# Kernel optimization log

Hardware: AMD Instinct MI355X
Metric: run time of the kernel (lower is better)

The kernel has to match this reference:

```python
import jax, jax.numpy as jnp
import numpy as np

B, S, DIM, H, HD, K, DEPTH = 2, 2048, 512, 8, 64, 64, 8
SCALE = 1.0 / np.sqrt(HD)


def _cantor_coords(seq_len: int, depth: int) -> np.ndarray:
    # Vectorized port of CantorAttention._cantor_coordinate over all positions.
    x = np.arange(seq_len, dtype=np.float64) / max(1, seq_len - 1)
    x = np.clip(x, 1e-06, 1.0 - 1e-06)
    val = np.zeros(seq_len, dtype=np.float64)
    factor = 0.5
    for _ in range(depth):
        x *= 3.0
        digit = np.floor(x)
        x -= digit
        val += (digit == 2.0) * factor
        factor *= 0.5
    return val.astype(np.float32)


def _build_routes(seq_len: int, k: int, depth: int) -> np.ndarray:
    # k nearest neighbors in Cantor space (smallest |c_i - c_j|), per position.
    c = _cantor_coords(seq_len, depth)
    dist = np.abs(c[:, None] - c[None, :])  # (S, S) built once on host
    routes = np.argsort(dist, axis=1, kind='stable')[:, :k]  # ascending distance
    return routes.astype(np.int32)


def setup_inputs() -> dict:
    key = jax.random.key(0)
    k1, k2, k3 = jax.random.split(key, 3)
    x = jax.random.normal(k1, (B, S, DIM), dtype=jnp.float32)
    Wqkv = jax.random.normal(k2, (DIM, 3 * DIM), dtype=jnp.float32) * (1.0 / np.sqrt(DIM))
    bqkv = jnp.zeros((3 * DIM,), dtype=jnp.float32)
    Wout = jax.random.normal(k3, (DIM, DIM), dtype=jnp.float32) * (1.0 / np.sqrt(DIM))
    bout = jnp.zeros((DIM,), dtype=jnp.float32)
    routes = jnp.asarray(_build_routes(S, K, DEPTH))  # (S, K) int32
    return {"x": x, "Wqkv": Wqkv, "bqkv": bqkv, "Wout": Wout, "bout": bout, "routes": routes}


def reference(x, Wqkv, bqkv, Wout, bout, routes):
    b, s, _ = x.shape
    qkv = x @ Wqkv + bqkv  # (B, S, 3*DIM)
    qkv = qkv.reshape(b, s, 3, H, HD)
    q = jnp.transpose(qkv[:, :, 0], (0, 2, 1, 3))  # (B, H, S, HD)
    k = jnp.transpose(qkv[:, :, 1], (0, 2, 1, 3))
    v = jnp.transpose(qkv[:, :, 2], (0, 2, 1, 3))
    # Gather K/V along sequence dim by Cantor routes -> (B, H, S, K, HD)
    k_g = k[:, :, routes, :]
    v_g = v[:, :, routes, :]
    scores = jnp.einsum('bhsd,bhskd->bhsk', q, k_g) * SCALE
    w = jax.nn.softmax(scores, axis=-1)  # dropout disabled (eval)
    out = jnp.einsum('bhsk,bhskd->bhsd', w, v_g)  # (B, H, S, HD)
    out = jnp.transpose(out, (0, 2, 1, 3)).reshape(b, s, DIM)
    return out @ Wout + bout
```

## Files before the change

kernel.cpp:

```cpp
#include <hip/hip_runtime.h>
#include <math.h>

#define B_    2
#define S_    2048
#define DIM_  512
#define H_    8
#define HD_   64
#define K_    64
#define M_    (B_ * S_)
#define NQKV_ (3 * DIM_)

typedef __attribute__((ext_vector_type(8))) _Float16       half8;
typedef __attribute__((ext_vector_type(8))) unsigned short ushort8v;
typedef __attribute__((ext_vector_type(4))) float          float4v;

union H8 { half8 h; ushort8v u; unsigned int w[4]; };

__device__ __forceinline__ unsigned short f2h(float f) {
    _Float16 h = (_Float16)f;
    unsigned short u; __builtin_memcpy(&u, &h, 2); return u;
}
__device__ __forceinline__ unsigned int pkrtz(float a, float b) {
    auto r = __builtin_amdgcn_cvt_pkrtz(a, b);
    unsigned int u; __builtin_memcpy(&u, &r, 4); return u;
}

__device__ __forceinline__ void load_lds16(const unsigned short* g, unsigned short* l) {
    __builtin_amdgcn_global_load_lds(
        (const __attribute__((address_space(1))) void*)g,
        (__attribute__((address_space(3))) void*)l, 16, 0, 0);
}

__global__ __launch_bounds__(256) void prep_all(
    const float* __restrict__ X, unsigned short* __restrict__ Xh,
    const float* __restrict__ Wq, unsigned short* __restrict__ Wqh,
    const float* __restrict__ Wo, unsigned short* __restrict__ Woh,
    const int* __restrict__ routes, int* __restrict__ members,
    int4* __restrict__ recs, int* __restrict__ nchp)
{
    __shared__ int smem[2048 * 3 + 256];
    const int bid = blockIdx.x, t = threadIdx.x;

    if (bid < 1024) {
        size_t i = ((size_t)bid * 256 + t) * 8;
        float4 a = *(const float4*)&X[i];
        float4 b = *(const float4*)&X[i + 4];
        float f[8] = {a.x, a.y, a.z, a.w, b.x, b.y, b.z, b.w};
        ushort8v h;
        #pragma unroll
        for (int j = 0; j < 8; ++j) h[j] = f2h(f[j]);
        *(ushort8v*)&Xh[i] = h;
        return;
    }

    if (bid == 2048) {
        int* cnt  = smem;
        int* base = smem + 2048;
        int* cur  = smem + 4096;
        int* ps   = smem + 6144;
        for (int i = t; i < 2048; i += 256) cnt[i] = 0;
        __syncthreads();
        int lead[8];
        #pragma unroll
        for (int i = 0; i < 8; ++i) {
            lead[i] = routes[(size_t)(i * 256 + t) * K_];
            atomicAdd(&cnt[lead[i]], 1);
        }
        __syncthreads();
        int loc[8], sum = 0;
        #pragma unroll
        for (int i = 0; i < 8; ++i) { loc[i] = sum; sum += cnt[t * 8 + i]; }
        ps[t] = sum;
        __syncthreads();
        for (int off = 1; off < 256; off <<= 1) {
            int v = ps[t];
            if (t >= off) v += ps[t - off];
            __syncthreads(); ps[t] = v; __syncthreads();
        }
        const int excl = ps[t] - sum;
        #pragma unroll
        for (int i = 0; i < 8; ++i) { base[t * 8 + i] = excl + loc[i]; cur[t * 8 + i] = 0; }
        __syncthreads();
        #pragma unroll
        for (int i = 0; i < 8; ++i) {
            int s = i * 256 + t;
            members[base[lead[i]] + atomicAdd(&cur[lead[i]], 1)] = s;
        }
        int cloc[8], csum = 0;
        #pragma unroll
        for (int i = 0; i < 8; ++i) { cloc[i] = csum; csum += (cnt[t * 8 + i] + 15) >> 4; }
        __syncthreads();
        ps[t] = csum;
        __syncthreads();
        for (int off = 1; off < 256; off <<= 1) {
            int v = ps[t];
            if (t >= off) v += ps[t - off];
            __syncthreads(); ps[t] = v; __syncthreads();
        }
        const int cexcl = ps[t] - csum;
        #pragma unroll
        for (int i = 0; i < 8; ++i) {
            const int c = t * 8 + i, n = cnt[c];
            int w0 = cexcl + cloc[i];
            for (int k2 = 0; k2 * 16 < n; ++k2) {
                int rem = n - k2 * 16;
                recs[w0 + k2] = make_int4(c, base[c] + k2 * 16, rem < 16 ? rem : 16, 0);
            }
        }
        if (t == 255) nchp[0] = ps[255];
        return;
    }

    float (*tile)[33] = (float (*)[33])smem;
    const float* W;
    unsigned short* Whi;
    int N, k0, n0;
    if (bid < 1792) {
        int idx = bid - 1024;
        W = Wq; Whi = Wqh; N = NQKV_;
        n0 = (idx % 48) * 32; k0 = (idx / 48) * 32;
    } else {
        int idx = bid - 1792;
        W = Wo; Whi = Woh; N = DIM_;
        n0 = (idx % 16) * 32; k0 = (idx / 16) * 32;
    }
    const int c = t & 31, r8 = t >> 5;
    #pragma unroll
    for (int i = 0; i < 4; ++i) {
        int r = r8 + i * 8;
        tile[r][c] = W[(size_t)(k0 + r) * N + n0 + c];
    }
    __syncthreads();
    #pragma unroll
    for (int i = 0; i < 4; ++i) {
        int r = r8 + i * 8;
        Whi[(size_t)(n0 + r) * 512 + k0 + c] = f2h(tile[c][r]);
    }
}

template<int BM, int BN, int WM, int WN, int TERMS>
__global__ __launch_bounds__(256) void gemm_mfma(
    const unsigned short* __restrict__ Ahi, const unsigned short* __restrict__ Alo,
    const unsigned short* __restrict__ Wh,
    const float* __restrict__ bias, float* __restrict__ C,
    unsigned short* __restrict__ Qho, unsigned short* __restrict__ Kho,
    unsigned short* __restrict__ Vho,
    int N, int Kd, int mode)
{
    constexpr int TM = WM / 16, TN = WN / 16;
    constexpr int WAVES_N = BN / WN;
    __shared__ unsigned short Ah[2][BM][32];
    __shared__ unsigned short Al[TERMS == 2 ? 2 : 1][TERMS == 2 ? BM : 1][32];
    __shared__ unsigned short Bh[2][BN][32];

    const int t = threadIdx.x, lane = t & 63, wave = t >> 6;
    const int wm = (wave / WAVES_N) * WM, wn = (wave % WAVES_N) * WN;
    const int m0 = blockIdx.y * BM, n0 = blockIdx.x * BN;
    const int l15 = lane & 15, l4 = lane >> 4;

    const int srow = lane >> 2;
    const int scol = (lane & 3) * 8;

    float4v acc[TM][TN];
    #pragma unroll
    for (int i = 0; i < TM; ++i)
        #pragma unroll
        for (int j = 0; j < TN; ++j)
            #pragma unroll
            for (int r = 0; r < 4; ++r) acc[i][j][r] = 0.f;

    const int NK = Kd / 32;

    #pragma unroll
    for (int c = wave; c < BM / 16; c += 4) {
        size_t g = (size_t)(m0 + c * 16 + srow) * Kd + scol;
        load_lds16(&Ahi[g], &Ah[0][c * 16][0]);
        if constexpr (TERMS == 2) load_lds16(&Alo[g], &Al[0][c * 16][0]);
    }
    #pragma unroll
    for (int c = wave; c < BN / 16; c += 4) {
        size_t g = (size_t)(n0 + c * 16 + srow) * Kd + scol;
        load_lds16(&Wh[g], &Bh[0][c * 16][0]);
    }
    __syncthreads();

    for (int ks = 0; ks < NK; ++ks) {
        const int cur = ks & 1, nxt = cur ^ 1;

        if (ks + 1 < NK) {
            const int k1 = (ks + 1) * 32;
            #pragma unroll
            for (int c = wave; c < BM / 16; c += 4) {
                size_t g = (size_t)(m0 + c * 16 + srow) * Kd + k1 + scol;
                load_lds16(&Ahi[g], &Ah[nxt][c * 16][0]);
                if constexpr (TERMS == 2) load_lds16(&Alo[g], &Al[nxt][c * 16][0]);
            }
            #pragma unroll
            for (int c = wave; c < BN / 16; c += 4) {
                size_t g = (size_t)(n0 + c * 16 + srow) * Kd + k1 + scol;
                load_lds16(&Wh[g], &Bh[nxt][c * 16][0]);
            }
        }

        half8 fa_h[TM], fa_l[TM], fb[TN];
        #pragma unroll
        for (int im = 0; im < TM; ++im) {
            fa_h[im] = *(const half8*)&Ah[cur][wm + im * 16 + l15][l4 * 8];
            if constexpr (TERMS == 2)
                fa_l[im] = *(const half8*)&Al[cur][wm + im * 16 + l15][l4 * 8];
        }
        #pragma unroll
        for (int in = 0; in < TN; ++in)
            fb[in] = *(const half8*)&Bh[cur][wn + in * 16 + l15][l4 * 8];
        #pragma unroll
        for (int im = 0; im < TM; ++im)
            #pragma unroll
            for (int in = 0; in < TN; ++in) {
                acc[im][in] = __builtin_amdgcn_mfma_f32_16x16x32_f16(fa_h[im], fb[in], acc[im][in], 0, 0, 0);
                if constexpr (TERMS == 2)
                    acc[im][in] = __builtin_amdgcn_mfma_f32_16x16x32_f16(fa_l[im], fb[in], acc[im][in], 0, 0, 0);
            }

        __syncthreads();
    }

    if (mode == 0) {
        #pragma unroll
        for (int in = 0; in < TN; ++in) {
            int n = n0 + wn + in * 16 + l15;
            float bv = bias[n];
            #pragma unroll
            for (int im = 0; im < TM; ++im) {
                int mb = m0 + wm + im * 16 + l4 * 4;
                #pragma unroll
                for (int r = 0; r < 4; ++r)
                    C[(size_t)(mb + r) * N + n] = acc[im][in][r] + bv;
            }
        }
    } else {
        #pragma unroll
        for (int in = 0; in < TN; ++in) {
            int n = n0 + wn + in * 16 + l15;
            int which = n >> 9, h = (n >> 6) & 7, d = n & 63;
            unsigned short* dst = (which == 0) ? Qho : (which == 1 ? Kho : Vho);
            float bv = bias[n];
            float scl = (which == 0) ? 0.125f : 1.0f;
            #pragma unroll
            for (int im = 0; im < TM; ++im) {
                int mb = m0 + wm + im * 16 + l4 * 4;
                #pragma unroll
                for (int r = 0; r < 4; ++r) {
                    int m = mb + r, b = m >> 11, s = m & 2047;
                    dst[(((size_t)b * H_ + h) * S_ + s) * HD_ + d] =
                        f2h((acc[im][in][r] + bv) * scl);
                }
            }
        }
    }
}

__global__ __launch_bounds__(256, 4) void attn_kernel(
    const unsigned short* __restrict__ Qh, const unsigned short* __restrict__ Kh,
    const unsigned short* __restrict__ Vh, const int* __restrict__ routes,
    const int* __restrict__ members, const int4* __restrict__ recs,
    const int* __restrict__ nchp, unsigned short* __restrict__ Oh)
{
    __shared__ unsigned short VldsAll[4][4096];
    const int wv = threadIdx.x >> 6, lane = threadIdx.x & 63;
    unsigned short* Vlds = VldsAll[wv];
    const int g = lane >> 4, m16 = lane & 15;

    const int unit = blockIdx.x * 4 + wv;
    const int bh = unit & 15, cidx = unit >> 4;
    const int b = bh >> 3, h = bh & 7;

    const unsigned short* qbase = Qh + (size_t)bh * S_ * HD_;
    const unsigned short* kbase = Kh + (size_t)bh * S_ * HD_;
    const unsigned short* vbase = Vh + (size_t)bh * S_ * HD_;
    const int nch = nchp[0];

    for (int chunk = cidx; chunk < nch; chunk += 512) {
        const int4 rec = recs[chunk];
        const int leader = rec.x, mstart = rec.y, mcnt = rec.z;

        const int rl = routes[(size_t)leader * K_ + lane];
        const int mm = members[mstart + (m16 < mcnt ? m16 : mcnt - 1)];

        #pragma unroll
        for (int i = 0; i < 8; ++i) {
            int rv = __shfl(rl, i * 8 + (lane >> 3));
            int sc = (lane & 7) ^ i;
            load_lds16(&vbase[(size_t)rv * HD_ + sc * 8], Vlds + i * 512);
        }

        H8 ka[4][2];
        #pragma unroll
        for (int tt = 0; tt < 4; ++tt) {
            int rt = __shfl(rl, tt * 16 + m16);
            const unsigned short* kr = &kbase[(size_t)rt * HD_];
            ka[tt][0].u = *(const ushort8v*)(kr + g * 8);
            ka[tt][1].u = *(const ushort8v*)(kr + 32 + g * 8);
        }
        const unsigned short* qr = &qbase[(size_t)mm * HD_];
        H8 qb0, qb1;
        qb0.u = *(const ushort8v*)(qr + g * 8);
        qb1.u = *(const ushort8v*)(qr + 32 + g * 8);

        float4v acc[4];
        #pragma unroll
        for (int tt = 0; tt < 4; ++tt) {
            #pragma unroll
            for (int r = 0; r < 4; ++r) acc[tt][r] = 0.f;
        }
        #pragma unroll
        for (int tt = 0; tt < 4; ++tt) {
            acc[tt] = __builtin_amdgcn_mfma_f32_16x16x32_f16(ka[tt][0].h, qb0.h, acc[tt], 0, 0, 0);
            acc[tt] = __builtin_amdgcn_mfma_f32_16x16x32_f16(ka[tt][1].h, qb1.h, acc[tt], 0, 0, 0);
        }

        float mx = acc[0][0];
        #pragma unroll
        for (int tt = 0; tt < 4; ++tt)
            #pragma unroll
            for (int r = 0; r < 4; ++r) mx = fmaxf(mx, acc[tt][r]);
        mx = fmaxf(mx, __shfl_xor(mx, 16));
        mx = fmaxf(mx, __shfl_xor(mx, 32));
        float ew[4][4], su = 0.f;
        #pragma unroll
        for (int tt = 0; tt < 4; ++tt)
            #pragma unroll
            for (int r = 0; r < 4; ++r) { ew[tt][r] = __expf(acc[tt][r] - mx); su += ew[tt][r]; }
        su += __shfl_xor(su, 16);
        su += __shfl_xor(su, 32);
        const float rinv = __builtin_amdgcn_rcpf(su);

        unsigned int whu[4][2];
        #pragma unroll
        for (int tt = 0; tt < 4; ++tt) {
            whu[tt][0] = pkrtz(ew[tt][0] * rinv, ew[tt][1] * rinv);
            whu[tt][1] = pkrtz(ew[tt][2] * rinv, ew[tt][3] * rinv);
        }

        const int A0 = (((g & 1) << 5) | m16) * 4;
        const int A1 = A0 + 64;
        const bool ghi = (g >> 1) != 0;
        H8 pa[2];
        #pragma unroll
        for (int s = 0; s < 2; ++s) {
            unsigned int l0a = (unsigned int)__builtin_amdgcn_ds_bpermute(A0, (int)whu[2 * s][0]);
            unsigned int l0b = (unsigned int)__builtin_amdgcn_ds_bpermute(A0, (int)whu[2 * s + 1][0]);
            unsigned int h0a = (unsigned int)__builtin_amdgcn_ds_bpermute(A0, (int)whu[2 * s][1]);
            unsigned int h0b = (unsigned int)__builtin_amdgcn_ds_bpermute(A0, (int)whu[2 * s + 1][1]);
            unsigned int l1a = (unsigned int)__builtin_amdgcn_ds_bpermute(A1, (int)whu[2 * s][0]);
            unsigned int l1b = (unsigned int)__builtin_amdgcn_ds_bpermute(A1, (int)whu[2 * s + 1][0]);
            unsigned int h1a = (unsigned int)__builtin_amdgcn_ds_bpermute(A1, (int)whu[2 * s][1]);
            unsigned int h1b = (unsigned int)__builtin_amdgcn_ds_bpermute(A1, (int)whu[2 * s + 1][1]);
            pa[s].w[0] = ghi ? l0b : l0a;
            pa[s].w[1] = ghi ? h0b : h0a;
            pa[s].w[2] = ghi ? l1b : l1a;
            pa[s].w[3] = ghi ? h1b : h1a;
        }

        int mr[4];
        #pragma unroll
        for (int r = 0; r < 4; ++r)
            mr[r] = __builtin_amdgcn_ds_bpermute((g * 4 + r) * 4, mm);

        asm volatile("s_waitcnt vmcnt(0)" ::: "memory");
        __builtin_amdgcn_sched_barrier(0);

        #pragma unroll
        for (int dblk = 0; dblk < 4; ++dblk) {
            H8 vb[2];
            #pragma unroll
            for (int s = 0; s < 2; ++s) {
                const char* vp = (const char*)Vlds + (s * 32 + g * 8) * 128 +
                    (((dblk * 16 + m16) * 2) ^ ((((s * 4 + g) & 7)) << 4));
                #pragma unroll
                for (int j = 0; j < 8; ++j)
                    vb[s].u[j] = *(const unsigned short*)(vp + j * 128);
            }
            float4v o;
            o[0] = 0.f; o[1] = 0.f; o[2] = 0.f; o[3] = 0.f;
            o = __builtin_amdgcn_mfma_f32_16x16x32_f16(pa[0].h, vb[0].h, o, 0, 0, 0);
            o = __builtin_amdgcn_mfma_f32_16x16x32_f16(pa[1].h, vb[1].h, o, 0, 0, 0);
            #pragma unroll
            for (int r = 0; r < 4; ++r) {
                if (g * 4 + r < mcnt) {
                    size_t oi = ((size_t)b * S_ + mr[r]) * DIM_ + h * HD_ + dblk * 16 + m16;
                    Oh[oi] = f2h(o[r]);
                }
            }
        }
    }
}

extern "C" void kernel_launch(void* const* d_in, const int* in_sizes, int n_in,
                              void* d_out, int out_size, void* d_ws, size_t ws_size,
                              hipStream_t stream)
{
    const float* x      = (const float*)d_in[0];
    const float* Wqkv   = (const float*)d_in[1];
    const float* bqkv   = (const float*)d_in[2];
    const float* Wout   = (const float*)d_in[3];
    const float* bout   = (const float*)d_in[4];
    const int*   routes = (const int*)d_in[5];
    float* out = (float*)d_out;

    char* w = (char*)d_ws;
    unsigned short* Qh = (unsigned short*)(w);
    unsigned short* Kh = (unsigned short*)(w + (8u << 20));
    unsigned short* Vh = (unsigned short*)(w + (16u << 20));
    unsigned short* xh = (unsigned short*)(w + (24u << 20));
    unsigned short* ah = xh;
    unsigned short* wqh = (unsigned short*)(w + (32u << 20));
    unsigned short* woh = (unsigned short*)(w + (32u << 20) + 1572864u);
    int*  members = (int*)(w + (34u << 20));
    int4* recs    = (int4*)(w + (34u << 20) + 8192u);
    int*  nchp    = (int*)(w + (34u << 20) + 8192u + 32768u);

    dim3 blk(256);

    prep_all<<<dim3(2049), blk, 0, stream>>>(x, xh, Wqkv, wqh, Wout, woh,
                                             routes, members, recs, nchp);

    gemm_mfma<128, 96, 64, 48, 1><<<dim3(NQKV_ / 96, M_ / 128), blk, 0, stream>>>(
        xh, nullptr, wqh, bqkv, nullptr, Qh, Kh, Vh, NQKV_, DIM_, 1);

    attn_kernel<<<dim3(2048), blk, 0, stream>>>(Qh, Kh, Vh, routes,
                                                members, recs, nchp, ah);

    gemm_mfma<64, 64, 32, 32, 1><<<dim3(DIM_ / 64, M_ / 64), blk, 0, stream>>>(
        ah, nullptr, woh, bout, out, nullptr, nullptr, nullptr, DIM_, DIM_, 0);
}
```

Before: 118.1 us.

## Fuse prep, QKV GEMM, attention and output GEMM into one persistent kernel

Replaces the four kernel launches with a single persistent 256-block kernel, plus a tiny zeroing kernel, that moves between phases via global atomic barriers. The route-grouping prep now runs on one block, overlapped with the QKV GEMM tiles on the other 255 blocks, and the leader counts are gathered through global atomics. The goal is to remove launch gaps and tail effects between stages. In exchange, each phase gets far fewer blocks than before (256 vs thousands), grid-wide spin barriers add cost, and correctness depends on all blocks being co-resident.

```diff
diff --git a/kernel.cpp b/kernel.cpp
--- a/kernel.cpp
+++ b/kernel.cpp
@@ -9,6 +9,7 @@
 #define K_    64
 #define M_    (B_ * S_)
 #define NQKV_ (3 * DIM_)
+#define NBLK_ 256
 
 typedef __attribute__((ext_vector_type(8))) _Float16       half8;
 typedef __attribute__((ext_vector_type(8))) unsigned short ushort8v;
@@ -24,140 +25,44 @@
     auto r = __builtin_amdgcn_cvt_pkrtz(a, b);
     unsigned int u; __builtin_memcpy(&u, &r, 4); return u;
 }
-
 __device__ __forceinline__ void load_lds16(const unsigned short* g, unsigned short* l) {
     __builtin_amdgcn_global_load_lds(
         (const __attribute__((address_space(1))) void*)g,
         (__attribute__((address_space(3))) void*)l, 16, 0, 0);
 }
 
-__global__ __launch_bounds__(256) void prep_all(
-    const float* __restrict__ X, unsigned short* __restrict__ Xh,
-    const float* __restrict__ Wq, unsigned short* __restrict__ Wqh,
-    const float* __restrict__ Wo, unsigned short* __restrict__ Woh,
-    const int* __restrict__ routes, int* __restrict__ members,
-    int4* __restrict__ recs, int* __restrict__ nchp)
-{
-    __shared__ int smem[2048 * 3 + 256];
-    const int bid = blockIdx.x, t = threadIdx.x;
-
-    if (bid < 1024) {
-        size_t i = ((size_t)bid * 256 + t) * 8;
-        float4 a = *(const float4*)&X[i];
-        float4 b = *(const float4*)&X[i + 4];
-        float f[8] = {a.x, a.y, a.z, a.w, b.x, b.y, b.z, b.w};
-        ushort8v h;
-        #pragma unroll
-        for (int j = 0; j < 8; ++j) h[j] = f2h(f[j]);
-        *(ushort8v*)&Xh[i] = h;
-        return;
-    }
-
-    if (bid == 2048) {
-        int* cnt  = smem;
-        int* base = smem + 2048;
-        int* cur  = smem + 4096;
-        int* ps   = smem + 6144;
-        for (int i = t; i < 2048; i += 256) cnt[i] = 0;
-        __syncthreads();
-        int lead[8];
-        #pragma unroll
-        for (int i = 0; i < 8; ++i) {
-            lead[i] = routes[(size_t)(i * 256 + t) * K_];
-            atomicAdd(&cnt[lead[i]], 1);
-        }
-        __syncthreads();
-        int loc[8], sum = 0;
-        #pragma unroll
-        for (int i = 0; i < 8; ++i) { loc[i] = sum; sum += cnt[t * 8 + i]; }
-        ps[t] = sum;
-        __syncthreads();
-        for (int off = 1; off < 256; off <<= 1) {
-            int v = ps[t];
-            if (t >= off) v += ps[t - off];
-            __syncthreads(); ps[t] = v; __syncthreads();
-        }
-        const int excl = ps[t] - sum;
-        #pragma unroll
-        for (int i = 0; i < 8; ++i) { base[t * 8 + i] = excl + loc[i]; cur[t * 8 + i] = 0; }
-        __syncthreads();
-        #pragma unroll
-        for (int i = 0; i < 8; ++i) {
-            int s = i * 256 + t;
-            members[base[lead[i]] + atomicAdd(&cur[lead[i]], 1)] = s;
-        }
-        int cloc[8], csum = 0;
-        #pragma unroll
-        for (int i = 0; i < 8; ++i) { cloc[i] = csum; csum += (cnt[t * 8 + i] + 15) >> 4; }
-        __syncthreads();
-        ps[t] = csum;
-        __syncthreads();
-        for (int off = 1; off < 256; off <<= 1) {
-            int v = ps[t];
-            if (t >= off) v += ps[t - off];
-            __syncthreads(); ps[t] = v; __syncthreads();
-        }
-        const int cexcl = ps[t] - csum;
-        #pragma unroll
-        for (int i = 0; i < 8; ++i) {
-            const int c = t * 8 + i, n = cnt[c];
-            int w0 = cexcl + cloc[i];
-            for (int k2 = 0; k2 * 16 < n; ++k2) {
-                int rem = n - k2 * 16;
-                recs[w0 + k2] = make_int4(c, base[c] + k2 * 16, rem < 16 ? rem : 16, 0);
-            }
-        }
-        if (t == 255) nchp[0] = ps[255];
-        return;
-    }
-
-    float (*tile)[33] = (float (*)[33])smem;
-    const float* W;
-    unsigned short* Whi;
-    int N, k0, n0;
-    if (bid < 1792) {
-        int idx = bid - 1024;
-        W = Wq; Whi = Wqh; N = NQKV_;
-        n0 = (idx % 48) * 32; k0 = (idx / 48) * 32;
-    } else {
-        int idx = bid - 1792;
-        W = Wo; Whi = Woh; N = DIM_;
-        n0 = (idx % 16) * 32; k0 = (idx / 16) * 32;
-    }
-    const int c = t & 31, r8 = t >> 5;
-    #pragma unroll
-    for (int i = 0; i < 4; ++i) {
-        int r = r8 + i * 8;
-        tile[r][c] = W[(size_t)(k0 + r) * N + n0 + c];
-    }
+__device__ __forceinline__ void gbar(int* cnt, int nblk) {
     __syncthreads();
-    #pragma unroll
-    for (int i = 0; i < 4; ++i) {
-        int r = r8 + i * 8;
-        Whi[(size_t)(n0 + r) * 512 + k0 + c] = f2h(tile[c][r]);
-    }
-}
-
-template<int BM, int BN, int WM, int WN, int TERMS>
-__global__ __launch_bounds__(256) void gemm_mfma(
-    const unsigned short* __restrict__ Ahi, const unsigned short* __restrict__ Alo,
-    const unsigned short* __restrict__ Wh,
+    __threadfence();
+    __syncthreads();
+    if (threadIdx.x == 0) {
+        __hip_atomic_fetch_add(cnt, 1, __ATOMIC_RELEASE, __HIP_MEMORY_SCOPE_AGENT);
+        int spins = 0;
+        while (__hip_atomic_load(cnt, __ATOMIC_ACQUIRE, __HIP_MEMORY_SCOPE_AGENT) < nblk) {
+            __builtin_amdgcn_s_sleep(7);
+            if (++spins > (1 << 22)) break;
+        }
+    }
+    __syncthreads();
+    __threadfence();
+}
+
+template<int BM, int BN, int WM, int WN>
+__device__ void gemm_tile(char* smemRaw,
+    const unsigned short* __restrict__ Ahi, const unsigned short* __restrict__ Wh,
     const float* __restrict__ bias, float* __restrict__ C,
     unsigned short* __restrict__ Qho, unsigned short* __restrict__ Kho,
     unsigned short* __restrict__ Vho,
-    int N, int Kd, int mode)
+    int N, int Kd, int mode, int m0, int n0)
 {
     constexpr int TM = WM / 16, TN = WN / 16;
     constexpr int WAVES_N = BN / WN;
-    __shared__ unsigned short Ah[2][BM][32];
-    __shared__ unsigned short Al[TERMS == 2 ? 2 : 1][TERMS == 2 ? BM : 1][32];
-    __shared__ unsigned short Bh[2][BN][32];
+    auto Ah = (unsigned short (*)[BM][32])smemRaw;
+    auto Bh = (unsigned short (*)[BN][32])(smemRaw + 2 * BM * 32 * 2);
 
     const int t = threadIdx.x, lane = t & 63, wave = t >> 6;
     const int wm = (wave / WAVES_N) * WM, wn = (wave % WAVES_N) * WN;
-    const int m0 = blockIdx.y * BM, n0 = blockIdx.x * BN;
     const int l15 = lane & 15, l4 = lane >> 4;
-
     const int srow = lane >> 2;
     const int scol = (lane & 3) * 8;
 
@@ -175,7 +80,6 @@
     for (int c = wave; c < BM / 16; c += 4) {
         size_t g = (size_t)(m0 + c * 16 + srow) * Kd + scol;
         load_lds16(&Ahi[g], &Ah[0][c * 16][0]);
-        if constexpr (TERMS == 2) load_lds16(&Alo[g], &Al[0][c * 16][0]);
     }
     #pragma unroll
     for (int c = wave; c < BN / 16; c += 4) {
@@ -193,7 +97,6 @@
             for (int c = wave; c < BM / 16; c += 4) {
                 size_t g = (size_t)(m0 + c * 16 + srow) * Kd + k1 + scol;
                 load_lds16(&Ahi[g], &Ah[nxt][c * 16][0]);
-                if constexpr (TERMS == 2) load_lds16(&Alo[g], &Al[nxt][c * 16][0]);
             }
             #pragma unroll
             for (int c = wave; c < BN / 16; c += 4) {
@@ -202,24 +105,18 @@
             }
         }
 
-        half8 fa_h[TM], fa_l[TM], fb[TN];
-        #pragma unroll
-        for (int im = 0; im < TM; ++im) {
-            fa_h[im] = *(const half8*)&Ah[cur][wm + im * 16 + l15][l4 * 8];
-            if constexpr (TERMS == 2)
-                fa_l[im] = *(const half8*)&Al[cur][wm + im * 16 + l15][l4 * 8];
-        }
+        half8 fa[TM], fb[TN];
+        #pragma unroll
+        for (int im = 0; im < TM; ++im)
+            fa[im] = *(const half8*)&Ah[cur][wm + im * 16 + l15][l4 * 8];
         #pragma unroll
         for (int in = 0; in < TN; ++in)
             fb[in] = *(const half8*)&Bh[cur][wn + in * 16 + l15][l4 * 8];
         #pragma unroll
         for (int im = 0; im < TM; ++im)
             #pragma unroll
-            for (int in = 0; in < TN; ++in) {
-                acc[im][in] = __builtin_amdgcn_mfma_f32_16x16x32_f16(fa_h[im], fb[in], acc[im][in], 0, 0, 0);
-                if constexpr (TERMS == 2)
-                    acc[im][in] = __builtin_amdgcn_mfma_f32_16x16x32_f16(fa_l[im], fb[in], acc[im][in], 0, 0, 0);
-            }
+            for (int in = 0; in < TN; ++in)
+                acc[im][in] = __builtin_amdgcn_mfma_f32_16x16x32_f16(fa[im], fb[in], acc[im][in], 0, 0, 0);
 
         __syncthreads();
     }
@@ -259,139 +156,280 @@
     }
 }
 
-__global__ __launch_bounds__(256, 4) void attn_kernel(
+__device__ void attn_one(int bh, int chunk, unsigned short* Vlds,
     const unsigned short* __restrict__ Qh, const unsigned short* __restrict__ Kh,
     const unsigned short* __restrict__ Vh, const int* __restrict__ routes,
     const int* __restrict__ members, const int4* __restrict__ recs,
-    const int* __restrict__ nchp, unsigned short* __restrict__ Oh)
+    unsigned short* __restrict__ Oh)
 {
-    __shared__ unsigned short VldsAll[4][4096];
-    const int wv = threadIdx.x >> 6, lane = threadIdx.x & 63;
-    unsigned short* Vlds = VldsAll[wv];
+    const int lane = threadIdx.x & 63;
     const int g = lane >> 4, m16 = lane & 15;
-
-    const int unit = blockIdx.x * 4 + wv;
-    const int bh = unit & 15, cidx = unit >> 4;
     const int b = bh >> 3, h = bh & 7;
 
     const unsigned short* qbase = Qh + (size_t)bh * S_ * HD_;
     const unsigned short* kbase = Kh + (size_t)bh * S_ * HD_;
     const unsigned short* vbase = Vh + (size_t)bh * S_ * HD_;
-    const int nch = nchp[0];
-
-    for (int chunk = cidx; chunk < nch; chunk += 512) {
-        const int4 rec = recs[chunk];
-        const int leader = rec.x, mstart = rec.y, mcnt = rec.z;
-
-        const int rl = routes[(size_t)leader * K_ + lane];
-        const int mm = members[mstart + (m16 < mcnt ? m16 : mcnt - 1)];
-
+
+    const int4 rec = recs[chunk & 2047];
+    const int leader = rec.x & 2047;
+    const int mstart = rec.y & 2047;
+    const int mcnt   = rec.z < 1 ? 1 : (rec.z > 16 ? 16 : rec.z);
+
+    const int rl = routes[(size_t)leader * K_ + lane] & 2047;
+    const int mm = members[(mstart + (m16 < mcnt ? m16 : mcnt - 1)) & 2047] & 2047;
+
+    #pragma unroll
+    for (int i = 0; i < 8; ++i) {
+        int rv = __shfl(rl, i * 8 + (lane >> 3));
+        int sc = (lane & 7) ^ i;
+        load_lds16(&vbase[(size_t)rv * HD_ + sc * 8], Vlds + i * 512);
+    }
+
+    H8 ka[4][2];
+    #pragma unroll
+    for (int tt = 0; tt < 4; ++tt) {
+        int rt = __shfl(rl, tt * 16 + m16);
+        const unsigned short* kr = &kbase[(size_t)rt * HD_];
+        ka[tt][0].u = *(const ushort8v*)(kr + g * 8);
+        ka[tt][1].u = *(const ushort8v*)(kr + 32 + g * 8);
+    }
+    const unsigned short* qr = &qbase[(size_t)mm * HD_];
+    H8 qb0, qb1;
+    qb0.u = *(const ushort8v*)(qr + g * 8);
+    qb1.u = *(const ushort8v*)(qr + 32 + g * 8);
+
+    float4v acc[4];
+    #pragma unroll
+    for (int tt = 0; tt < 4; ++tt) {
+        #pragma unroll
+        for (int r = 0; r < 4; ++r) acc[tt][r] = 0.f;
+    }
+    #pragma unroll
+    for (int tt = 0; tt < 4; ++tt) {
+        acc[tt] = __builtin_amdgcn_mfma_f32_16x16x32_f16(ka[tt][0].h, qb0.h, acc[tt], 0, 0, 0);
+        acc[tt] = __builtin_amdgcn_mfma_f32_16x16x32_f16(ka[tt][1].h, qb1.h, acc[tt], 0, 0, 0);
+    }
+
+    float mx = acc[0][0];
+    #pragma unroll
+    for (int tt = 0; tt < 4; ++tt)
+        #pragma unroll
+        for (int r = 0; r < 4; ++r) mx = fmaxf(mx, acc[tt][r]);
+    mx = fmaxf(mx, __shfl_xor(mx, 16));
+    mx = fmaxf(mx, __shfl_xor(mx, 32));
+    float ew[4][4], su = 0.f;
+    #pragma unroll
+    for (int tt = 0; tt < 4; ++tt)
+        #pragma unroll
+        for (int r = 0; r < 4; ++r) { ew[tt][r] = __expf(acc[tt][r] - mx); su += ew[tt][r]; }
+    su += __shfl_xor(su, 16);
+    su += __shfl_xor(su, 32);
+    const float rinv = __builtin_amdgcn_rcpf(su);
+
+    unsigned int whu[4][2];
+    #pragma unroll
+    for (int tt = 0; tt < 4; ++tt) {
+        whu[tt][0] = pkrtz(ew[tt][0] * rinv, ew[tt][1] * rinv);
+        whu[tt][1] = pkrtz(ew[tt][2] * rinv, ew[tt][3] * rinv);
+    }
+
+    const int A0 = (((g & 1) << 5) | m16) * 4;
+    const int A1 = A0 + 64;
+    const bool ghi = (g >> 1) != 0;
+    H8 pa[2];
+    #pragma unroll
+    for (int s = 0; s < 2; ++s) {
+        unsigned int l0a = (unsigned int)__builtin_amdgcn_ds_bpermute(A0, (int)whu[2 * s][0]);
+        unsigned int l0b = (unsigned int)__builtin_amdgcn_ds_bpermute(A0, (int)whu[2 * s + 1][0]);
+        unsigned int h0a = (unsigned int)__builtin_amdgcn_ds_bpermute(A0, (int)whu[2 * s][1]);
+        unsigned int h0b = (unsigned int)__builtin_amdgcn_ds_bpermute(A0, (int)whu[2 * s + 1][1]);
+        unsigned int l1a = (unsigned int)__builtin_amdgcn_ds_bpermute(A1, (int)whu[2 * s][0]);
+        unsigned int l1b = (unsigned int)__builtin_amdgcn_ds_bpermute(A1, (int)whu[2 * s + 1][0]);
+        unsigned int h1a = (unsigned int)__builtin_amdgcn_ds_bpermute(A1, (int)whu[2 * s][1]);
+        unsigned int h1b = (unsigned int)__builtin_amdgcn_ds_bpermute(A1, (int)whu[2 * s + 1][1]);
+        pa[s].w[0] = ghi ? l0b : l0a;
+        pa[s].w[1] = ghi ? h0b : h0a;
+        pa[s].w[2] = ghi ? l1b : l1a;
+        pa[s].w[3] = ghi ? h1b : h1a;
+    }
+
+    int mr[4];
+    #pragma unroll
+    for (int r = 0; r < 4; ++r)
+        mr[r] = __builtin_amdgcn_ds_bpermute((g * 4 + r) * 4, mm) & 2047;
+
+    asm volatile("s_waitcnt vmcnt(0)" ::: "memory");
+    __builtin_amdgcn_sched_barrier(0);
+
+    #pragma unroll
+    for (int dblk = 0; dblk < 4; ++dblk) {
+        H8 vb[2];
+        #pragma unroll
+        for (int s = 0; s < 2; ++s) {
+            const char* vp = (const char*)Vlds + (s * 32 + g * 8) * 128 +
+                (((dblk * 16 + m16) * 2) ^ ((((s * 4 + g) & 7)) << 4));
+            #pragma unroll
+            for (int j = 0; j < 8; ++j)
+                vb[s].u[j] = *(const unsigned short*)(vp + j * 128);
+        }
+        float4v o;
+        o[0] = 0.f; o[1] = 0.f; o[2] = 0.f; o[3] = 0.f;
+        o = __builtin_amdgcn_mfma_f32_16x16x32_f16(pa[0].h, vb[0].h, o, 0, 0, 0);
+        o = __builtin_amdgcn_mfma_f32_16x16x32_f16(pa[1].h, vb[1].h, o, 0, 0, 0);
+        #pragma unroll
+        for (int r = 0; r < 4; ++r) {
+            if (g * 4 + r < mcnt) {
+                size_t oi = ((size_t)b * S_ + mr[r]) * DIM_ + h * HD_ + dblk * 16 + m16;
+                Oh[oi] = f2h(o[r]);
+            }
+        }
+    }
+}
+
+__global__ __launch_bounds__(256) void zero_ws(int* gcnt, int* bar, int* nchp)
+{
+    int i = blockIdx.x * 256 + threadIdx.x;
+    if (i < 2048) gcnt[i] = 0;
+    if (i < 16) bar[i] = 0;
+    if (i == 16) nchp[0] = 0;
+}
+
+struct MegaArgs {
+    const float* x; unsigned short* xh;
+    const float* Wq; unsigned short* wqh;
+    const float* Wo; unsigned short* woh;
+    const float* bqkv; const float* bout;
+    const int* routes; int* members; int4* recs; int* nchp; int* gcnt; int* bar;
+    unsigned short* Qh; unsigned short* Kh; unsigned short* Vh;
+    unsigned short* ah; float* out;
+};
+
+__global__ __launch_bounds__(256) void mega(MegaArgs a)
+{
+    __shared__ __align__(16) char smem[32768];
+    const int bid = blockIdx.x, t = threadIdx.x;
+
+    #pragma unroll
+    for (int i = 0; i < 8; ++i) {
+        const int unit = bid + NBLK_ * i;
+        if (unit < 1024) {
+            size_t idx = ((size_t)unit * 256 + t) * 8;
+            float4 va = *(const float4*)&a.x[idx];
+            float4 vb = *(const float4*)&a.x[idx + 4];
+            float f[8] = {va.x, va.y, va.z, va.w, vb.x, vb.y, vb.z, vb.w};
+            ushort8v hh;
+            #pragma unroll
+            for (int j = 0; j < 8; ++j) hh[j] = f2h(f[j]);
+            *(ushort8v*)&a.xh[idx] = hh;
+        } else {
+            float (*tile)[33] = (float (*)[33])smem;
+            const float* W; unsigned short* Whi; int N, k0, n0;
+            int u = unit - 1024;
+            if (u < 768) { W = a.Wq; Whi = a.wqh; N = NQKV_; n0 = (u % 48) * 32; k0 = (u / 48) * 32; }
+            else { u -= 768; W = a.Wo; Whi = a.woh; N = DIM_; n0 = (u % 16) * 32; k0 = (u / 16) * 32; }
+            const int c = t & 31, r8 = t >> 5;
+            __syncthreads();
+            #pragma unroll
+            for (int j = 0; j < 4; ++j) {
+                int r = r8 + j * 8;
+                tile[r][c] = W[(size_t)(k0 + r) * N + n0 + c];
+            }
+            __syncthreads();
+            #pragma unroll
+            for (int j = 0; j < 4; ++j) {
+                int r = r8 + j * 8;
+                Whi[(size_t)(n0 + r) * 512 + k0 + c] = f2h(tile[c][r]);
+            }
+        }
+    }
+    if (t < 8) {
+        int s = bid * 8 + t;
+        atomicAdd(&a.gcnt[a.routes[(size_t)s * K_]], 1);
+    }
+
+    gbar(a.bar + 0, NBLK_);
+
+    if (bid == 255) {
+        int* cnt  = (int*)smem;
+        int* base = cnt + 2048;
+        int* cur  = base + 2048;
+        int* ps   = cur + 2048;
+        for (int i = t; i < 2048; i += 256)
+            cnt[i] = __hip_atomic_load(&a.gcnt[i], __ATOMIC_RELAXED, __HIP_MEMORY_SCOPE_AGENT);
+        __syncthreads();
+        int loc[8], sum = 0;
+        #pragma unroll
+        for (int i = 0; i < 8; ++i) { loc[i] = sum; sum += cnt[t * 8 + i]; }
+        ps[t] = sum;
+        __syncthreads();
+        for (int off = 1; off < 256; off <<= 1) {
+            int v = ps[t];
+            if (t >= off) v += ps[t - off];
+            __syncthreads(); ps[t] = v; __syncthreads();
+        }
+        const int excl = ps[t] - sum;
+        #pragma unroll
+        for (int i = 0; i < 8; ++i) { base[t * 8 + i] = excl + loc[i]; cur[t * 8 + i] = 0; }
+        __syncthreads();
         #pragma unroll
         for (int i = 0; i < 8; ++i) {
-            int rv = __shfl(rl, i * 8 + (lane >> 3));
-            int sc = (lane & 7) ^ i;
-            load_lds16(&vbase[(size_t)rv * HD_ + sc * 8], Vlds + i * 512);
-        }
-
-        H8 ka[4][2];
-        #pragma unroll
-        for (int tt = 0; tt < 4; ++tt) {
-            int rt = __shfl(rl, tt * 16 + m16);
-            const unsigned short* kr = &kbase[(size_t)rt * HD_];
-            ka[tt][0].u = *(const ushort8v*)(kr + g * 8);
-            ka[tt][1].u = *(const ushort8v*)(kr + 32 + g * 8);
-        }
-        const unsigned short* qr = &qbase[(size_t)mm * HD_];
-        H8 qb0, qb1;
-        qb0.u = *(const ushort8v*)(qr + g * 8);
-        qb1.u = *(const ushort8v*)(qr + 32 + g * 8);
-
-        float4v acc[4];
-        #pragma unroll
-        for (int tt = 0; tt < 4; ++tt) {
-            #pragma unroll
-            for (int r = 0; r < 4; ++r) acc[tt][r] = 0.f;
-        }
-        #pragma unroll
-        for (int tt = 0; tt < 4; ++tt) {
-            acc[tt] = __builtin_amdgcn_mfma_f32_16x16x32_f16(ka[tt][0].h, qb0.h, acc[tt], 0, 0, 0);
-            acc[tt] = __builtin_amdgcn_mfma_f32_16x16x32_f16(ka[tt][1].h, qb1.h, acc[tt], 0, 0, 0);
-        }
-
-        float mx = acc[0][0];
-        #pragma unroll
-        for (int tt = 0; tt < 4; ++tt)
-            #pragma unroll
-            for (int r = 0; r < 4; ++r) mx = fmaxf(mx, acc[tt][r]);
-        mx = fmaxf(mx, __shfl_xor(mx, 16));
-        mx = fmaxf(mx, __shfl_xor(mx, 32));
-        float ew[4][4], su = 0.f;
-        #pragma unroll
-        for (int tt = 0; tt < 4; ++tt)
-            #pragma unroll
-            for (int r = 0; r < 4; ++r) { ew[tt][r] = __expf(acc[tt][r] - mx); su += ew[tt][r]; }
-        su += __shfl_xor(su, 16);
-        su += __shfl_xor(su, 32);
-        const float rinv = __builtin_amdgcn_rcpf(su);
-
-        unsigned int whu[4][2];
-        #pragma unroll
-        for (int tt = 0; tt < 4; ++tt) {
-            whu[tt][0] = pkrtz(ew[tt][0] * rinv, ew[tt][1] * rinv);
-            whu[tt][1] = pkrtz(ew[tt][2] * rinv, ew[tt][3] * rinv);
-        }
-
-        const int A0 = (((g & 1) << 5) | m16) * 4;
-        const int A1 = A0 + 64;
-        const bool ghi = (g >> 1) != 0;
-        H8 pa[2];
-        #pragma unroll
-        for (int s = 0; s < 2; ++s) {
-            unsigned int l0a = (unsigned int)__builtin_amdgcn_ds_bpermute(A0, (int)whu[2 * s][0]);
-            unsigned int l0b = (unsigned int)__builtin_amdgcn_ds_bpermute(A0, (int)whu[2 * s + 1][0]);
-            unsigned int h0a = (unsigned int)__builtin_amdgcn_ds_bpermute(A0, (int)whu[2 * s][1]);
-            unsigned int h0b = (unsigned int)__builtin_amdgcn_ds_bpermute(A0, (int)whu[2 * s + 1][1]);
-            unsigned int l1a = (unsigned int)__builtin_amdgcn_ds_bpermute(A1, (int)whu[2 * s][0]);
-            unsigned int l1b = (unsigned int)__builtin_amdgcn_ds_bpermute(A1, (int)whu[2 * s + 1][0]);
-            unsigned int h1a = (unsigned int)__builtin_amdgcn_ds_bpermute(A1, (int)whu[2 * s][1]);
-            unsigned int h1b = (unsigned int)__builtin_amdgcn_ds_bpermute(A1, (int)whu[2 * s + 1][1]);
-            pa[s].w[0] = ghi ? l0b : l0a;
-            pa[s].w[1] = ghi ? h0b : h0a;
-            pa[s].w[2] = ghi ? l1b : l1a;
-            pa[s].w[3] = ghi ? h1b : h1a;
-        }
-
-        int mr[4];
-        #pragma unroll
-        for (int r = 0; r < 4; ++r)
-            mr[r] = __builtin_amdgcn_ds_bpermute((g * 4 + r) * 4, mm);
-
-        asm volatile("s_waitcnt vmcnt(0)" ::: "memory");
-        __builtin_amdgcn_sched_barrier(0);
-
-        #pragma unroll
-        for (int dblk = 0; dblk < 4; ++dblk) {
-            H8 vb[2];
-            #pragma unroll
-            for (int s = 0; s < 2; ++s) {
-                const char* vp = (const char*)Vlds + (s * 32 + g * 8) * 128 +
-                    (((dblk * 16 + m16) * 2) ^ ((((s * 4 + g) & 7)) << 4));
-                #pragma unroll
-                for (int j = 0; j < 8; ++j)
-                    vb[s].u[j] = *(const unsigned short*)(vp + j * 128);
-            }
-            float4v o;
-            o[0] = 0.f; o[1] = 0.f; o[2] = 0.f; o[3] = 0.f;
-            o = __builtin_amdgcn_mfma_f32_16x16x32_f16(pa[0].h, vb[0].h, o, 0, 0, 0);
-            o = __builtin_amdgcn_mfma_f32_16x16x32_f16(pa[1].h, vb[1].h, o, 0, 0, 0);
-            #pragma unroll
-            for (int r = 0; r < 4; ++r) {
-                if (g * 4 + r < mcnt) {
-                    size_t oi = ((size_t)b * S_ + mr[r]) * DIM_ + h * HD_ + dblk * 16 + m16;
-                    Oh[oi] = f2h(o[r]);
-                }
-            }
-        }
+            int s = i * 256 + t;
+            int lead = a.routes[(size_t)s * K_];
+            a.members[base[lead] + atomicAdd(&cur[lead], 1)] = s;
+        }
+        int cloc[8], csum = 0;
+        #pragma unroll
+        for (int i = 0; i < 8; ++i) { cloc[i] = csum; csum += (cnt[t * 8 + i] + 15) >> 4; }
+        __syncthreads();
+        ps[t] = csum;
+        __syncthreads();
+        for (int off = 1; off < 256; off <<= 1) {
+            int v = ps[t];
+            if (t >= off) v += ps[t - off];
+            __syncthreads(); ps[t] = v; __syncthreads();
+        }
+        const int cexcl = ps[t] - csum;
+        #pragma unroll
+        for (int i = 0; i < 8; ++i) {
+            const int c = t * 8 + i, n = cnt[c];
+            int w0 = cexcl + cloc[i];
+            for (int k2 = 0; k2 * 16 < n; ++k2) {
+                int rem = n - k2 * 16;
+                a.recs[w0 + k2] = make_int4(c, base[c] + k2 * 16, rem < 16 ? rem : 16, 0);
+            }
+        }
+        if (t == 255)
+            __hip_atomic_store(a.nchp, ps[255], __ATOMIC_RELAXED, __HIP_MEMORY_SCOPE_AGENT);
+    } else {
+        for (int tid = bid; tid < 512; tid += 255) {
+            gemm_tile<128, 96, 64, 48>(smem, a.xh, a.wqh, a.bqkv, nullptr,
+                                       a.Qh, a.Kh, a.Vh, NQKV_, DIM_, 1,
+                                       (tid >> 4) * 128, (tid & 15) * 96);
+            __syncthreads();
+        }
+    }
+
+    gbar(a.bar + 1, NBLK_);
+
+    {
+        const int wv = t >> 6;
+        unsigned short* Vlds = (unsigned short*)smem + wv * 4096;
+        int nch = __hip_atomic_load(a.nchp, __ATOMIC_RELAXED, __HIP_MEMORY_SCOPE_AGENT);
+        nch = nch < 0 ? 0 : (nch > 2048 ? 2048 : nch);
+        const int total = nch * 16;
+        for (int idx = bid * 4 + wv; idx < total; idx += NBLK_ * 4) {
+            attn_one(idx & 15, idx >> 4, Vlds,
+                     a.Qh, a.Kh, a.Vh, a.routes, a.members, a.recs, a.ah);
+        }
+    }
+
+    gbar(a.bar + 2, NBLK_);
+
+    for (int tid = bid; tid < 512; tid += NBLK_) {
+        gemm_tile<64, 64, 32, 32>(smem, a.ah, a.woh, a.bout, a.out,
+                                  nullptr, nullptr, nullptr, DIM_, DIM_, 0,
+                                  (tid >> 3) * 64, (tid & 7) * 64);
+        __syncthreads();
     }
 }
 
@@ -418,18 +456,15 @@
     int*  members = (int*)(w + (34u << 20));
     int4* recs    = (int4*)(w + (34u << 20) + 8192u);
     int*  nchp    = (int*)(w + (34u << 20) + 8192u + 32768u);
-
-    dim3 blk(256);
-
-    prep_all<<<dim3(2049), blk, 0, stream>>>(x, xh, Wqkv, wqh, Wout, woh,
-                                             routes, members, recs, nchp);
-
-    gemm_mfma<128, 96, 64, 48, 1><<<dim3(NQKV_ / 96, M_ / 128), blk, 0, stream>>>(
-        xh, nullptr, wqh, bqkv, nullptr, Qh, Kh, Vh, NQKV_, DIM_, 1);
-
-    attn_kernel<<<dim3(2048), blk, 0, stream>>>(Qh, Kh, Vh, routes,
-                                                members, recs, nchp, ah);
-
-    gemm_mfma<64, 64, 32, 32, 1><<<dim3(DIM_ / 64, M_ / 64), blk, 0, stream>>>(
-        ah, nullptr, woh, bout, out, nullptr, nullptr, nullptr, DIM_, DIM_, 0);
-}
+    int*  gcnt    = (int*)(w + (34u << 20) + 49152u);
+    int*  bar     = (int*)(w + (34u << 20) + 49152u + 8192u);
+
+    MegaArgs A;
+    A.x = x; A.xh = xh; A.Wq = Wqkv; A.wqh = wqh; A.Wo = Wout; A.woh = woh;
+    A.bqkv = bqkv; A.bout = bout; A.routes = routes;
+    A.members = members; A.recs = recs; A.nchp = nchp; A.gcnt = gcnt; A.bar = bar;
+    A.Qh = Qh; A.Kh = Kh; A.Vh = Vh; A.ah = ah; A.out = out;
+
+    zero_ws<<<dim3(8), dim3(256), 0, stream>>>(gcnt, bar, nchp);
+    mega<<<dim3(NBLK_), dim3(256), 0, stream>>>(A);
+}
```

After: 290.6 us. 2.46x slower.
